# Performance work log

Measured on AMD Instinct MI355X. Metric: run time of the kernel, lower is better.

## Reference

```python
import jax, jax.numpy as jnp
import numpy as np
import math

B = 16
IMG = 224
P = 16
C_IN = 3
E = 768
H = 12
HD = E // H          # 64
D = 6                # depth
MLP = 3072
NC = 1000
GH = IMG // P        # 14
N = GH * GH + 1      # 197 tokens incl cls
LAMBDA_INIT = 0.8
EPS = 1e-5


def setup_inputs() -> dict:
    key = jax.random.key(0)
    ks = jax.random.split(key, 24)
    s = 0.02
    inp = {
        "x": jax.random.normal(ks[0], (B, C_IN, IMG, IMG), jnp.float32),
        "conv_w": jax.random.normal(ks[1], (E, C_IN, P, P), jnp.float32) * s,
        "conv_b": jnp.zeros((E,), jnp.float32),
        "cls_token": jax.random.normal(ks[2], (1, 1, E), jnp.float32) * s,
        "pos_embed": jax.random.normal(ks[3], (1, N, E), jnp.float32) * s,
        # per-layer stacked params (leading dim D)
        "Wq": jax.random.normal(ks[4], (D, E, 2 * E), jnp.float32) * s,
        "Wk": jax.random.normal(ks[5], (D, E, 2 * E), jnp.float32) * s,
        "Wv": jax.random.normal(ks[6], (D, E, 2 * E), jnp.float32) * s,
        "lq1": jax.random.normal(ks[7], (D, H, HD), jnp.float32) * 0.1,
        "lk1": jax.random.normal(ks[8], (D, H, HD), jnp.float32) * 0.1,
        "lq2": jax.random.normal(ks[9], (D, H, HD), jnp.float32) * 0.1,
        "lk2": jax.random.normal(ks[10], (D, H, HD), jnp.float32) * 0.1,
        "gn_g": jnp.ones((D, 2 * HD), jnp.float32),
        "gn_b": jnp.zeros((D, 2 * HD), jnp.float32),
        "Wo": jax.random.normal(ks[11], (D, 2 * E, E), jnp.float32) * s,
        "ln1_g": jnp.ones((D, E), jnp.float32),
        "ln1_b": jnp.zeros((D, E), jnp.float32),
        "ln2_g": jnp.ones((D, E), jnp.float32),
        "ln2_b": jnp.zeros((D, E), jnp.float32),
        "mlp_w1": jax.random.normal(ks[12], (D, E, MLP), jnp.float32) * s,
        "mlp_b1": jnp.zeros((D, MLP), jnp.float32),
        "mlp_w2": jax.random.normal(ks[13], (D, MLP, E), jnp.float32) * s,
        "mlp_b2": jnp.zeros((D, E), jnp.float32),
        "lnf_g": jnp.ones((E,), jnp.float32),
        "lnf_b": jnp.zeros((E,), jnp.float32),
        "head_w": jax.random.normal(ks[14], (E, NC), jnp.float32) * s,
        "head_b": jnp.zeros((NC,), jnp.float32),
    }
    return inp


def _ln(z, g, b):
    m = jnp.mean(z, axis=-1, keepdims=True)
    v = jnp.var(z, axis=-1, keepdims=True)
    return (z - m) * jax.lax.rsqrt(v + EPS) * g + b


def _forward(x, conv_w, conv_b, cls_token, pos_embed, Wq, Wk, Wv,
             lq1, lk1, lq2, lk2, gn_g, gn_b, Wo,
             ln1_g, ln1_b, ln2_g, ln2_b,
             mlp_w1, mlp_b1, mlp_w2, mlp_b2,
             lnf_g, lnf_b, head_w, head_b):
    Bx = x.shape[0]
    # patch embedding (conv stride=kernel == non-overlapping patch matmul)
    xp = x.reshape(Bx, C_IN, GH, P, GH, P)
    tok = jnp.einsum('bchpwq,ecpq->bhwe', xp, conv_w).reshape(Bx, GH * GH, E) + conv_b
    h = jnp.concatenate([jnp.broadcast_to(cls_token, (Bx, 1, E)), tok], axis=1) + pos_embed

    scale = 1.0 / math.sqrt(HD)

    def block(h, p):
        xn = _ln(h, p['ln1_g'], p['ln1_b'])
        q = (xn @ p['Wq']).reshape(Bx, N, H, 2 * HD).transpose(0, 2, 1, 3)
        k = (xn @ p['Wk']).reshape(Bx, N, H, 2 * HD).transpose(0, 2, 1, 3)
        v = (xn @ p['Wv']).reshape(Bx, N, H, 2 * HD).transpose(0, 2, 1, 3)
        q1, q2 = q[..., :HD], q[..., HD:]
        k1, k2 = k[..., :HD], k[..., HD:]
        a1 = jax.nn.softmax(jnp.einsum('bhnd,bhmd->bhnm', q1, k1) * scale, axis=-1)
        a2 = jax.nn.softmax(jnp.einsum('bhnd,bhmd->bhnm', q2, k2) * scale, axis=-1)
        lam = (jnp.exp(jnp.sum(p['lq1'] * p['lk1'], axis=-1))
               - jnp.exp(jnp.sum(p['lq2'] * p['lk2'], axis=-1)) + LAMBDA_INIT)  # (H,)
        attn = a1 - lam[None, :, None, None] * a2
        o = jnp.einsum('bhnm,bhmd->bhnd', attn, v)  # (B,H,N,2HD)
        # GroupNorm(1 group) over (N, 2HD) per (b,h) sample, per-channel affine
        m = jnp.mean(o, axis=(2, 3), keepdims=True)
        var = jnp.var(o, axis=(2, 3), keepdims=True)
        o = (o - m) * jax.lax.rsqrt(var + EPS) * p['gn_g'] + p['gn_b']
        o = o.transpose(0, 2, 1, 3).reshape(Bx, N, 2 * E) @ p['Wo']
        h = h + o
        xn2 = _ln(h, p['ln2_g'], p['ln2_b'])
        ff = jax.nn.gelu(xn2 @ p['mlp_w1'] + p['mlp_b1'], approximate=False) @ p['mlp_w2'] + p['mlp_b2']
        return h + ff, attn

    params = dict(Wq=Wq, Wk=Wk, Wv=Wv, lq1=lq1, lk1=lk1, lq2=lq2, lk2=lk2,
                  gn_g=gn_g, gn_b=gn_b, Wo=Wo, ln1_g=ln1_g, ln1_b=ln1_b,
                  ln2_g=ln2_g, ln2_b=ln2_b, mlp_w1=mlp_w1, mlp_b1=mlp_b1,
                  mlp_w2=mlp_w2, mlp_b2=mlp_b2)
    h, attns = jax.lax.scan(block, h, params)
    h = _ln(h, lnf_g, lnf_b)
    logits = h[:, 0] @ head_w + head_b
    return logits, attns  # attns: (D, B, H, N, N)


def reference(x, conv_w, conv_b, cls_token, pos_embed, Wq, Wk, Wv,
              lq1, lk1, lq2, lk2, gn_g, gn_b, Wo,
              ln1_g, ln1_b, ln2_g, ln2_b,
              mlp_w1, mlp_b1, mlp_w2, mlp_b2,
              lnf_g, lnf_b, head_w, head_b):
    return _forward(x, conv_w, conv_b, cls_token, pos_embed, Wq, Wk, Wv,
                    lq1, lk1, lq2, lk2, gn_g, gn_b, Wo,
                    ln1_g, ln1_b, ln2_g, ln2_b,
                    mlp_w1, mlp_b1, mlp_w2, mlp_b2,
                    lnf_g, lnf_b, head_w, head_b)
```

## Files before the change

### kernel.cpp

```cpp
#include <hip/hip_runtime.h>
#include <hip/hip_bf16.h>
#include <math.h>

#define BB 16
#define NT 197
#define EE 768
#define HH 12
#define E2 1536
#define MLPD 3072
#define NCLS 1000
#define ND 6
#define EPSF 1e-5f
#define SCALEF 0.125f
#define LAMINIT 0.8f
#define TOKC 3152

using v8bf  = __attribute__((ext_vector_type(8))) __bf16;
using f32x4 = __attribute__((ext_vector_type(4))) float;
typedef __hip_bfloat16 bf16;

#define AS1 __attribute__((address_space(1)))
#define AS3 __attribute__((address_space(3)))

__device__ __forceinline__ void gld16(const void* g, void* l) {
    __builtin_amdgcn_global_load_lds((const AS1 void*)g, (AS3 void*)l, 16, 0, 0);
}

__device__ __forceinline__ float gelu_f(float x) {
    const float u = x + 0.044715f * x * x * x;
    const float e = __expf(fminf(1.5957691216f * u, 80.f));
    return x * e / (e + 1.f);
}

__global__ __launch_bounds__(256) void gemm_bf16(
    const bf16* __restrict__ A, const bf16* __restrict__ Wt,
    const float* __restrict__ bias, float* __restrict__ C0,
    float* __restrict__ C1, float* __restrict__ C2,
    const float* __restrict__ pos, int M, int K, int ldA, int ldB, int Nc, int mode)
{
    __shared__ __align__(16) unsigned char smem[32768];
    const int t = threadIdx.x;
    const int wave = t >> 6, lane = t & 63;
    const int wr = wave >> 1, wc = wave & 1;
    const int lr = lane & 15, lk = lane >> 4;

    const int bid0 = blockIdx.y * gridDim.x + blockIdx.x;
    const int nwg = gridDim.x * gridDim.y;
    const int qv = nwg >> 3, rv = nwg & 7;
    const int xcd = bid0 & 7, ii = bid0 >> 3;
    const int wgid = (xcd < rv ? xcd * (qv + 1) : rv * (qv + 1) + (xcd - rv) * qv) + ii;
    const int rowBase = (wgid / gridDim.x) * 128;
    const int colBase = (wgid % gridDim.x) * 128;
    const size_t zoff = (size_t)blockIdx.z * K * 2;

    f32x4 acc[4][4];
#pragma unroll
    for (int i = 0; i < 4; ++i)
#pragma unroll
        for (int j = 0; j < 4; ++j) acc[i][j] = (f32x4){0.f,0.f,0.f,0.f};

    const size_t ldA2 = (size_t)ldA * 2, ldB2 = (size_t)ldB * 2;
    const int srow = t >> 3;
    const int schunk = (t & 7) ^ ((t >> 3) & 7);
    const char* Abase = (const char*)A + zoff + schunk * 16;
    const char* Bbase = (const char*)Wt + zoff + schunk * 16;
    unsigned char* lA = smem + t * 16;
    unsigned char* lB = smem + 16384 + t * 16;
    const v8bf* Sa = (const v8bf*)smem;
    const v8bf* Sb = (const v8bf*)(smem + 16384);

    int rA[4], rB[4];
#pragma unroll
    for (int c = 0; c < 4; ++c) {
        rA[c] = min(rowBase + c * 32 + srow, M - 1);
        rB[c] = colBase + c * 32 + srow;
    }

    for (int k0 = 0; k0 < K; k0 += 64) {
        const size_t kb = (size_t)k0 * 2;
#pragma unroll
        for (int c = 0; c < 4; ++c) {
            gld16(Abase + (size_t)rA[c] * ldA2 + kb, lA + c * 4096);
            gld16(Bbase + (size_t)rB[c] * ldB2 + kb, lB + c * 4096);
        }
        __syncthreads();
#pragma unroll
        for (int s = 0; s < 2; ++s) {
            const int xr_ = (s * 4 + lk) ^ (lr & 7);
            v8bf af[4], bfr[4];
#pragma unroll
            for (int i = 0; i < 4; ++i) af[i] = Sa[(wr * 64 + i * 16 + lr) * 8 + xr_];
#pragma unroll
            for (int j = 0; j < 4; ++j) bfr[j] = Sb[(wc * 64 + j * 16 + lr) * 8 + xr_];
#pragma unroll
            for (int i = 0; i < 4; ++i)
#pragma unroll
                for (int j = 0; j < 4; ++j)
                    acc[i][j] = __builtin_amdgcn_mfma_f32_16x16x32_bf16(af[i], bfr[j], acc[i][j], 0, 0, 0);
        }
        __syncthreads();
    }

    if (mode == 0) {
        float* Cs = (float*)smem;
        float* C0z = C0 + (size_t)blockIdx.z * M * Nc;
#pragma unroll
        for (int half = 0; half < 2; ++half) {
            __syncthreads();
            if (wr == half) {
#pragma unroll
                for (int i = 0; i < 4; ++i)
#pragma unroll
                    for (int j = 0; j < 4; ++j)
#pragma unroll
                        for (int rr = 0; rr < 4; ++rr)
                            Cs[(i*16 + lk*4 + rr)*128 + wc*64 + j*16 + lr] = acc[i][j][rr];
            }
            __syncthreads();
#pragma unroll
            for (int k = 0; k < 8; ++k) {
                const int idx = k*256 + t;
                const int row = idx >> 5, c4 = idx & 31;
                const int r = rowBase + half*64 + row;
                if (r < M)
                    *(float4*)&C0z[(size_t)r*Nc + colBase + c4*4] = *(float4*)&Cs[row*128 + c4*4];
            }
        }
    } else if (mode == 1) {
        const int which = colBase / E2;
        if (which == 2) {
#pragma unroll
            for (int i = 0; i < 4; ++i)
#pragma unroll
                for (int j = 0; j < 4; ++j)
#pragma unroll
                    for (int rr = 0; rr < 4; ++rr) {
                        const int r = rowBase + wr * 64 + i * 16 + lk * 4 + rr;
                        const int c = colBase + wc * 64 + j * 16 + lr;
                        if (r >= M) continue;
                        const int b_ = r / NT, n_ = r % NT;
                        const int cc = c % E2;
                        const int h_ = cc >> 7, d_ = cc & 127;
                        const size_t bh = (size_t)(b_ * HH + h_);
                        ((bf16*)C2)[((bh * 7 + (n_ >> 5)) * 8 + (d_ >> 4)) * 512 +
                                    (size_t)(((d_ & 15) + (((n_ >> 3) & 3) << 4)) * 8 + (n_ & 7))] =
                            __float2bfloat16(acc[i][j][rr]);
                    }
        } else {
            const int hFix = (colBase % E2) >> 7;
            bf16* dstBase = (bf16*)(which == 0 ? C0 : C1);
            bf16* Cs = (bf16*)smem;
            __syncthreads();
#pragma unroll
            for (int i = 0; i < 4; ++i)
#pragma unroll
                for (int j = 0; j < 4; ++j)
#pragma unroll
                    for (int rr = 0; rr < 4; ++rr)
                        Cs[(wr*64 + i*16 + lk*4 + rr)*128 + wc*64 + j*16 + lr] =
                            __float2bfloat16(acc[i][j][rr]);
            __syncthreads();
#pragma unroll
            for (int k = 0; k < 8; ++k) {
                const int idx = k*256 + t;
                const int row = idx >> 4, c8 = idx & 15;
                const int r = rowBase + row;
                if (r < M) {
                    const int b_ = r / NT, n_ = r - b_ * NT;
                    const size_t bh = (size_t)(b_ * HH + hFix);
                    *(uint4*)(dstBase + (bh * 208 + n_) * 128 + c8 * 8) =
                        *(uint4*)&Cs[row*128 + c8*8];
                }
            }
        }
    } else if (mode == 3) {
        bf16* Cs = (bf16*)smem;
        __syncthreads();
#pragma unroll
        for (int i = 0; i < 4; ++i)
#pragma unroll
            for (int j = 0; j < 4; ++j)
#pragma unroll
                for (int rr = 0; rr < 4; ++rr) {
                    const int c = colBase + wc*64 + j*16 + lr;
                    float val = acc[i][j][rr] + bias[c];
                    Cs[(wr*64 + i*16 + lk*4 + rr)*128 + wc*64 + j*16 + lr] =
                        __float2bfloat16(gelu_f(val));
                }
        __syncthreads();
        bf16* C0b = (bf16*)C0;
#pragma unroll
        for (int k = 0; k < 8; ++k) {
            const int idx = k*256 + t;
            const int row = idx >> 4, c8 = idx & 15;
            const int r = rowBase + row;
            if (r < M)
                *(uint4*)(C0b + (size_t)r*Nc + colBase + c8*8) = *(uint4*)&Cs[row*128 + c8*8];
        }
    } else {
#pragma unroll
        for (int i = 0; i < 4; ++i)
#pragma unroll
            for (int j = 0; j < 4; ++j)
#pragma unroll
                for (int rr = 0; rr < 4; ++rr) {
                    const int r = rowBase + wr * 64 + i * 16 + lk * 4 + rr;
                    const int c = colBase + wc * 64 + j * 16 + lr;
                    if (r >= M) continue;
                    const int b_ = r / 196, p_ = r % 196;
                    C0[((size_t)(b_ * NT) + 1 + p_) * EE + c] =
                        acc[i][j][rr] + bias[c] + pos[(size_t)(1 + p_) * EE + c];
                }
    }
}

__global__ __launch_bounds__(64) void attn_mfma(
    const bf16* __restrict__ Qrm, const bf16* __restrict__ Krm,
    const bf16* __restrict__ Vf, const float* __restrict__ lamp,
    float* __restrict__ aout, float* __restrict__ o, float* __restrict__ stats)
{
    const int lane = threadIdx.x;
    const int fid = blockIdx.x;
    const int xcd = fid & 7, rest = fid >> 3;
    const int qt = rest % 13, g = rest / 13;
    const int bh = g * 8 + xcd;
    const int hh = bh % HH;
    const int lr = lane & 15, lk = lane >> 4;

    __shared__ __align__(16) bf16 P[16][232];

    {
        const int r = lane & 15, c0 = 192 + (lane >> 4) * 10;
#pragma unroll
        for (int j = 0; j < 10; ++j) P[r][c0 + j] = __float2bfloat16(0.f);
    }

    v8bf qa[4];
    const bf16* Qb = Qrm + ((size_t)bh * 208 + qt * 16) * 128;
#pragma unroll
    for (int kk = 0; kk < 4; ++kk)
        qa[kk] = *(const v8bf*)(Qb + lr * 128 + kk * 32 + lk * 8);

    const bf16* Kb = Krm + (size_t)bh * 208 * 128;
    const f32x4 zf = {0.f, 0.f, 0.f, 0.f};
    f32x4 s1[13], s2[13];
#pragma unroll
    for (int t = 0; t < 13; ++t) {
        const bf16* Kt = Kb + (t * 16 + lr) * 128 + lk * 8;
        const v8bf k0 = *(const v8bf*)(Kt);
        const v8bf k1 = *(const v8bf*)(Kt + 32);
        const v8bf k2 = *(const v8bf*)(Kt + 64);
        const v8bf k3 = *(const v8bf*)(Kt + 96);
        s1[t] = __builtin_amdgcn_mfma_f32_16x16x32_bf16(qa[1], k1,
                __builtin_amdgcn_mfma_f32_16x16x32_bf16(qa[0], k0, zf, 0, 0, 0), 0, 0, 0);
        s2[t] = __builtin_amdgcn_mfma_f32_16x16x32_bf16(qa[3], k3,
                __builtin_amdgcn_mfma_f32_16x16x32_bf16(qa[2], k2, zf, 0, 0, 0), 0, 0, 0);
    }

    float m1[4] = {-1e30f,-1e30f,-1e30f,-1e30f}, m2[4] = {-1e30f,-1e30f,-1e30f,-1e30f};
#pragma unroll
    for (int t = 0; t < 13; ++t) {
        const bool kv = (t * 16 + lr) < NT;
#pragma unroll
        for (int rr = 0; rr < 4; ++rr) {
            s1[t][rr] = kv ? s1[t][rr] * SCALEF : -1e30f;
            s2[t][rr] = kv ? s2[t][rr] * SCALEF : -1e30f;
            m1[rr] = fmaxf(m1[rr], s1[t][rr]);
            m2[rr] = fmaxf(m2[rr], s2[t][rr]);
        }
    }
#pragma unroll
    for (int off = 8; off >= 1; off >>= 1)
#pragma unroll
        for (int rr = 0; rr < 4; ++rr) {
            m1[rr] = fmaxf(m1[rr], __shfl_xor(m1[rr], off));
            m2[rr] = fmaxf(m2[rr], __shfl_xor(m2[rr], off));
        }

    float z1[4] = {0,0,0,0}, z2[4] = {0,0,0,0};
#pragma unroll
    for (int t = 0; t < 13; ++t)
#pragma unroll
        for (int rr = 0; rr < 4; ++rr) {
            const float e1 = __expf(s1[t][rr] - m1[rr]);
            const float e2 = __expf(s2[t][rr] - m2[rr]);
            s1[t][rr] = e1; s2[t][rr] = e2;
            z1[rr] += e1; z2[rr] += e2;
        }
#pragma unroll
    for (int off = 8; off >= 1; off >>= 1)
#pragma unroll
        for (int rr = 0; rr < 4; ++rr) {
            z1[rr] += __shfl_xor(z1[rr], off);
            z2[rr] += __shfl_xor(z2[rr], off);
        }
    const float lam = lamp[hh];
    float r1[4], r2[4];
#pragma unroll
    for (int rr = 0; rr < 4; ++rr) { r1[rr] = 1.f / z1[rr]; r2[rr] = lam / z2[rr]; }

    __syncthreads();
#pragma unroll
    for (int t = 0; t < 13; ++t) {
        const int m_ = t * 16 + lr;
#pragma unroll
        for (int rr = 0; rr < 4; ++rr) {
            const float p = s1[t][rr] * r1[rr] - s2[t][rr] * r2[rr];
            const int n_ = lk * 4 + rr;
            P[n_][m_] = __float2bfloat16(p);
            const int n_g = qt * 16 + n_;
            if (m_ < NT && n_g < NT)
                aout[((size_t)bh * NT + n_g) * NT + m_] = p;
        }
    }
    __syncthreads();

    f32x4 oacc[8];
#pragma unroll
    for (int dt = 0; dt < 8; ++dt) oacc[dt] = zf;
    const v8bf* Vp = (const v8bf*)(Vf + (size_t)bh * 7 * 8 * 512);
    const bf16* Pb = &P[0][0];
#pragma unroll
    for (int mk = 0; mk < 7; ++mk) {
        const v8bf pa = *(const v8bf*)(Pb + lr * 232 + mk * 32 + lk * 8);
#pragma unroll
        for (int dt = 0; dt < 8; ++dt)
            oacc[dt] = __builtin_amdgcn_mfma_f32_16x16x32_bf16(
                pa, Vp[(mk * 8 + dt) * 64 + lane], oacc[dt], 0, 0, 0);
    }
#pragma unroll
    for (int dt = 0; dt < 8; ++dt)
#pragma unroll
        for (int rr = 0; rr < 4; ++rr) {
            const int n_g = qt * 16 + lk * 4 + rr;
            if (n_g < NT)
                o[((size_t)bh * NT + n_g) * 128 + dt * 16 + lr] = oacc[dt][rr];
        }

    float s = 0.f, ss = 0.f;
#pragma unroll
    for (int dt = 0; dt < 8; ++dt)
#pragma unroll
        for (int rr = 0; rr < 4; ++rr) {
            const int n_g = qt * 16 + lk * 4 + rr;
            const float vv = (n_g < NT) ? oacc[dt][rr] : 0.f;
            s += vv; ss += vv * vv;
        }
#pragma unroll
    for (int off = 32; off >= 1; off >>= 1) {
        s  += __shfl_xor(s, off);
        ss += __shfl_xor(ss, off);
    }
    if (lane == 0) {
        stats[(bh * 13 + qt) * 2]     = s;
        stats[(bh * 13 + qt) * 2 + 1] = ss;
    }
}

__global__ __launch_bounds__(256) void gn_apply(
    const float* __restrict__ o, const float* __restrict__ stats,
    const float* __restrict__ g, const float* __restrict__ bb, bf16* __restrict__ o2)
{
    const int bh = blockIdx.y, qq = blockIdx.x;
    const int t = threadIdx.x;
    float S = 0.f, SS = 0.f;
#pragma unroll
    for (int j = 0; j < 13; ++j) {
        S  += stats[(bh * 13 + j) * 2];
        SS += stats[(bh * 13 + j) * 2 + 1];
    }
    const float inv = 1.f / (float)(NT * 128);
    const float mean = S * inv;
    const float var  = SS * inv - mean * mean;
    const float rstd = rsqrtf(var + EPSF);
    const int b_ = bh / HH, h_ = bh % HH;
    const float4* ob = (const float4*)(o + (size_t)bh * NT * 128);
    const float4* g4 = (const float4*)g;
    const float4* b4 = (const float4*)bb;
    for (int idx = t; idx < 50 * 32; idx += 256) {
        const int n_ = qq * 50 + (idx >> 5);
        if (n_ >= NT) continue;
        const int d4 = idx & 31;
        const float4 v4 = ob[n_ * 32 + d4];
        const float4 gg = g4[d4], bv = b4[d4];
        bf16 tmp[4];
        tmp[0] = __float2bfloat16((v4.x - mean) * rstd * gg.x + bv.x);
        tmp[1] = __float2bfloat16((v4.y - mean) * rstd * gg.y + bv.y);
        tmp[2] = __float2bfloat16((v4.z - mean) * rstd * gg.z + bv.z);
        tmp[3] = __float2bfloat16((v4.w - mean) * rstd * gg.w + bv.w);
        *(uint2*)(o2 + ((size_t)(b_ * NT + n_)) * E2 + h_ * 128 + d4 * 4) = *(uint2*)tmp;
    }
}

__global__ __launch_bounds__(256) void ln_rows(
    const float* __restrict__ in, const float* __restrict__ g,
    const float* __restrict__ bb, bf16* __restrict__ out)
{
    const int r = blockIdx.x;
    const int t = threadIdx.x;
    const float* x = in + (size_t)r * EE;
    const float v0 = x[t], v1 = x[t+256], v2 = x[t+512];
    __shared__ float rs[256], rss[256];
    rs[t]  = v0+v1+v2;
    rss[t] = v0*v0+v1*v1+v2*v2;
    __syncthreads();
    for (int st = 128; st > 0; st >>= 1) {
        if (t < st) { rs[t] += rs[t+st]; rss[t] += rss[t+st]; }
        __syncthreads();
    }
    const float mean = rs[0] * (1.f/768.f);
    const float var  = rss[0] * (1.f/768.f) - mean*mean;
    const float rstd = rsqrtf(var + EPSF);
    bf16* o = out + (size_t)r * EE;
    o[t]     = __float2bfloat16((v0-mean)*rstd*g[t]     + bb[t]);
    o[t+256] = __float2bfloat16((v1-mean)*rstd*g[t+256] + bb[t+256]);
    o[t+512] = __float2bfloat16((v2-mean)*rstd*g[t+512] + bb[t+512]);
}

__global__ __launch_bounds__(192) void ln_fuse(
    const float* __restrict__ hin, const float* __restrict__ Pp,
    const float* __restrict__ bias, const float* __restrict__ g,
    const float* __restrict__ bb, float* __restrict__ hout, bf16* __restrict__ xout)
{
    const int r = blockIdx.x;
    const int t = threadIdx.x;
    const int lane = t & 63, wv = t >> 6;
    const size_t base4 = (size_t)r * 192 + t;
    float4 v = ((const float4*)hin)[base4];
    const float4 p0 = ((const float4*)Pp)[base4];
    const float4 p1 = ((const float4*)Pp)[(size_t)TOKC * 192 + base4];
    v.x += p0.x + p1.x; v.y += p0.y + p1.y; v.z += p0.z + p1.z; v.w += p0.w + p1.w;
    if (bias) {
        const float4 bv = ((const float4*)bias)[t];
        v.x += bv.x; v.y += bv.y; v.z += bv.z; v.w += bv.w;
    }
    float s  = v.x + v.y + v.z + v.w;
    float ss = v.x*v.x + v.y*v.y + v.z*v.z + v.w*v.w;
#pragma unroll
    for (int off = 32; off >= 1; off >>= 1) {
        s  += __shfl_xor(s, off);
        ss += __shfl_xor(ss, off);
    }
    __shared__ float ws_[3][2];
    if (lane == 0) { ws_[wv][0] = s; ws_[wv][1] = ss; }
    __syncthreads();
    const float S  = ws_[0][0] + ws_[1][0] + ws_[2][0];
    const float SS = ws_[0][1] + ws_[1][1] + ws_[2][1];
    const float mean = S * (1.f/768.f);
    const float var  = SS * (1.f/768.f) - mean*mean;
    const float rstd = rsqrtf(var + EPSF);
    ((float4*)hout)[base4] = v;
    const float4 gg = ((const float4*)g)[t];
    const float4 bv2 = ((const float4*)bb)[t];
    bf16 tmp[4];
    tmp[0] = __float2bfloat16((v.x-mean)*rstd*gg.x + bv2.x);
    tmp[1] = __float2bfloat16((v.y-mean)*rstd*gg.y + bv2.y);
    tmp[2] = __float2bfloat16((v.z-mean)*rstd*gg.z + bv2.z);
    tmp[3] = __float2bfloat16((v.w-mean)*rstd*gg.w + bv2.w);
    *(uint2*)(xout + base4 * 4) = *(uint2*)tmp;
}

__global__ void lam_kernel(const float* __restrict__ lq1, const float* __restrict__ lk1,
                           const float* __restrict__ lq2, const float* __restrict__ lk2,
                           float* __restrict__ lam)
{
    const int i = threadIdx.x;
    if (i < ND*HH) {
        float d1 = 0.f, d2 = 0.f;
        for (int d = 0; d < 64; ++d) {
            d1 += lq1[i*64+d]*lk1[i*64+d];
            d2 += lq2[i*64+d]*lk2[i*64+d];
        }
        lam[i] = expf(d1) - expf(d2) + LAMINIT;
    }
}

__global__ void cls_kernel(const float* __restrict__ cls, const float* __restrict__ pos,
                           float* __restrict__ h)
{
    const int i = blockIdx.x*256 + threadIdx.x;
    if (i < BB*EE) {
        const int b_ = i / EE, e_ = i % EE;
        h[(size_t)(b_*NT)*EE + e_] = cls[e_] + pos[e_];
    }
}

__global__ void im2col_kernel(const float* __restrict__ x, bf16* __restrict__ xcol)
{
    const int i = blockIdx.x*256 + threadIdx.x;
    if (i >= 3136*EE) return;
    const int kidx = i % EE;
    const int p_ = i / EE;
    const int b_ = p_ / 196;
    const int pp = p_ % 196;
    const int gh = pp / 14, gw = pp % 14;
    const int c_ = kidx >> 8, rr = (kidx >> 4) & 15, q_ = kidx & 15;
    xcol[i] = __float2bfloat16(x[((size_t)(b_*3 + c_)*224 + gh*16 + rr)*224 + gw*16 + q_]);
}

__global__ void convert_flat(const float* __restrict__ in, bf16* __restrict__ out, int n)
{
    const int i = blockIdx.x*256 + threadIdx.x;
    if (i < n) out[i] = __float2bfloat16(in[i]);
}

__global__ void transpose_pack(const float* __restrict__ Wq, const float* __restrict__ Wk,
                               const float* __restrict__ Wv, const float* __restrict__ Wo,
                               const float* __restrict__ W1, const float* __restrict__ W2,
                               bf16* __restrict__ wall)
{
    __shared__ float tile[64][65];
    int bid = blockIdx.x;
    const int dl = bid / 2304; bid -= dl * 2304;
    bf16* wq_t = wall + (size_t)dl * 9437184;
    bf16* wo_t = wq_t + 3538944;
    bf16* w1_t = wo_t + 1179648;
    bf16* w2_t = w1_t + 2359296;
    const float* src; bf16* dst; int K, N, gx;
    if (bid < 864) {
        const int z = bid / 288; bid -= z * 288;
        src = (z == 0 ? Wq : (z == 1 ? Wk : Wv)) + (size_t)dl * EE * E2;
        dst = wq_t + (size_t)z * E2 * EE; K = EE; N = E2; gx = 24;
    } else if (bid < 1152) { src = Wo + (size_t)dl*E2*EE; dst = wo_t; K = E2; N = EE; gx = 12; bid -= 864; }
    else if (bid < 1728)   { src = W1 + (size_t)dl*EE*MLPD; dst = w1_t; K = EE; N = MLPD; gx = 48; bid -= 1152; }
    else                   { src = W2 + (size_t)dl*MLPD*EE; dst = w2_t; K = MLPD; N = EE; gx = 12; bid -= 1728; }
    const int bx = bid % gx, by = bid / gx;
    const int t = threadIdx.x;
    const int n0 = bx*64, k0 = by*64;
    {
        const int c4 = t & 15, kr = t >> 4;
#pragma unroll
        for (int i = 0; i < 4; ++i) {
            const int row = i * 16 + kr;
            const float4 v = *(const float4*)(src + (size_t)(k0 + row) * N + n0 + c4 * 4);
            tile[row][c4*4+0] = v.x; tile[row][c4*4+1] = v.y;
            tile[row][c4*4+2] = v.z; tile[row][c4*4+3] = v.w;
        }
    }
    __syncthreads();
    {
        const int ko = t & 7, nb = t >> 3;
#pragma unroll
        for (int i = 0; i < 2; ++i) {
            const int n = i * 32 + nb;
            bf16 tmp[8];
#pragma unroll
            for (int j = 0; j < 8; ++j)
                tmp[j] = __float2bfloat16(tile[ko*8+j][n]);
            *(uint4*)(dst + (size_t)(n0 + n) * K + k0 + ko * 8) = *(uint4*)tmp;
        }
    }
}

__global__ __launch_bounds__(256) void ln_cls(
    const float* __restrict__ h, const float* __restrict__ g,
    const float* __restrict__ bb, float* __restrict__ xr)
{
    const int b_ = blockIdx.x;
    const int t = threadIdx.x;
    const float* x = h + (size_t)(b_*NT)*EE;
    const float v0 = x[t], v1 = x[t+256], v2 = x[t+512];
    __shared__ float rs[256], rss[256];
    rs[t]  = v0+v1+v2;
    rss[t] = v0*v0+v1*v1+v2*v2;
    __syncthreads();
    for (int st = 128; st > 0; st >>= 1) {
        if (t < st) { rs[t] += rs[t+st]; rss[t] += rss[t+st]; }
        __syncthreads();
    }
    const float mean = rs[0] * (1.f/768.f);
    const float var  = rss[0] * (1.f/768.f) - mean*mean;
    const float rstd = rsqrtf(var + EPSF);
    float* o = xr + (size_t)b_ * EE;
    o[t]     = (v0-mean)*rstd*g[t]     + bb[t];
    o[t+256] = (v1-mean)*rstd*g[t+256] + bb[t+256];
    o[t+512] = (v2-mean)*rstd*g[t+512] + bb[t+512];
}

__global__ __launch_bounds__(256) void head_gemm(
    const float* __restrict__ xr, const float* __restrict__ hw,
    const float* __restrict__ hb, float* __restrict__ logits)
{
    const int b_ = blockIdx.y, ct = blockIdx.x;
    const int t = threadIdx.x;
    const int c_loc = t & 63, kp = t >> 6;
    const int c = ct * 64 + c_loc;
    __shared__ float xs[768];
    for (int i = t; i < 768; i += 256) xs[i] = xr[(size_t)b_*EE + i];
    __syncthreads();
    float acc = 0.f;
    if (c < NCLS) {
        const int k0 = kp * 192;
        for (int kk = k0; kk < k0 + 192; ++kk)
            acc += xs[kk] * hw[(size_t)kk * NCLS + c];
    }
    __shared__ float red[4][64];
    red[kp][c_loc] = acc;
    __syncthreads();
    if (kp == 0 && c < NCLS)
        logits[(size_t)b_*NCLS + c] =
            red[0][c_loc] + red[1][c_loc] + red[2][c_loc] + red[3][c_loc] + hb[c];
}

extern "C" void kernel_launch(void* const* d_in, const int* in_sizes, int n_in,
                              void* d_out, int out_size, void* d_ws, size_t ws_size,
                              hipStream_t stream)
{
    const float* x      = (const float*)d_in[0];
    const float* conv_w = (const float*)d_in[1];
    const float* conv_b = (const float*)d_in[2];
    const float* cls    = (const float*)d_in[3];
    const float* pos    = (const float*)d_in[4];
    const float* Wq     = (const float*)d_in[5];
    const float* Wk     = (const float*)d_in[6];
    const float* Wv     = (const float*)d_in[7];
    const float* lq1    = (const float*)d_in[8];
    const float* lk1    = (const float*)d_in[9];
    const float* lq2    = (const float*)d_in[10];
    const float* lk2    = (const float*)d_in[11];
    const float* gn_g   = (const float*)d_in[12];
    const float* gn_b   = (const float*)d_in[13];
    const float* Wo     = (const float*)d_in[14];
    const float* ln1_g  = (const float*)d_in[15];
    const float* ln1_b  = (const float*)d_in[16];
    const float* ln2_g  = (const float*)d_in[17];
    const float* ln2_b  = (const float*)d_in[18];
    const float* mlp_w1 = (const float*)d_in[19];
    const float* mlp_b1 = (const float*)d_in[20];
    const float* mlp_w2 = (const float*)d_in[21];
    const float* mlp_b2 = (const float*)d_in[22];
    const float* lnf_g  = (const float*)d_in[23];
    const float* lnf_b  = (const float*)d_in[24];
    const float* head_w = (const float*)d_in[25];
    const float* head_b = (const float*)d_in[26];

    float* out_f    = (float*)d_out;
    float* logits   = out_f;
    float* attn_out = out_f + (size_t)BB*NCLS;

    const int TOK = TOKC;
    const size_t TOKE = (size_t)TOK*EE;

    float* ws   = (float*)d_ws;
    float* h    = ws;
    float* o    = h + TOKE;
    float* Pp   = o + (size_t)BB*HH*NT*128;
    bf16*  Qrm  = (bf16*)(Pp + 2*TOKE);
    bf16*  Krm  = Qrm + (size_t)192*208*128;
    bf16*  Vf   = Krm + (size_t)192*208*128;
    bf16*  act2 = Vf + (size_t)192*7*8*512;
    bf16*  xn   = act2 + (size_t)TOK*MLPD;
    bf16*  wall = xn + TOKE;
    bf16*  cwbf = wall + (size_t)6*9437184;
    float* lam  = (float*)(cwbf + (size_t)EE*EE);
    float* xr   = lam + 128;
    float* gnst = xr + (size_t)BB*EE;

    hipMemsetAsync(Vf, 0, (size_t)192*7*8*512*2, stream);

    lam_kernel<<<1, 128, 0, stream>>>(lq1, lk1, lq2, lk2, lam);
    convert_flat<<<(EE*EE+255)/256, 256, 0, stream>>>(conv_w, cwbf, EE*EE);
    transpose_pack<<<6*2304, 256, 0, stream>>>(Wq, Wk, Wv, Wo, mlp_w1, mlp_w2, wall);
    im2col_kernel<<<(3136*EE+255)/256, 256, 0, stream>>>(x, xn);
    cls_kernel<<<(BB*EE+255)/256, 256, 0, stream>>>(cls, pos, h);
    gemm_bf16<<<dim3(EE/128, 25), 256, 0, stream>>>(
        xn, cwbf, conv_b, h, nullptr, nullptr, pos, 3136, EE, EE, EE, EE, 4);

    ln_rows<<<TOK, 256, 0, stream>>>(h, ln1_g, ln1_b, xn);

    for (int dl = 0; dl < ND; ++dl) {
        bf16* wq_t = wall + (size_t)dl*9437184;
        bf16* wo_t = wq_t + 3538944;
        bf16* w1_t = wo_t + 1179648;
        bf16* w2_t = w1_t + 2359296;

        gemm_bf16<<<dim3(4608/128, 25), 256, 0, stream>>>(
            xn, wq_t, nullptr, (float*)Qrm, (float*)Krm, (float*)Vf, nullptr,
            TOK, EE, EE, EE, 4608, 1);
        attn_mfma<<<2496, 64, 0, stream>>>(
            Qrm, Krm, Vf, lam + dl*HH, attn_out + (size_t)dl*BB*HH*NT*NT, o, gnst);
        gn_apply<<<dim3(4, BB*HH), 256, 0, stream>>>(
            o, gnst, gn_g + dl*128, gn_b + dl*128, act2);
        gemm_bf16<<<dim3(EE/128, 25, 2), 256, 0, stream>>>(
            act2, wo_t, nullptr, Pp, nullptr, nullptr, nullptr,
            TOK, E2/2, E2, E2, EE, 0);
        ln_fuse<<<TOK, 192, 0, stream>>>(
            h, Pp, nullptr, ln2_g + dl*EE, ln2_b + dl*EE, h, xn);
        gemm_bf16<<<dim3(MLPD/128, 25), 256, 0, stream>>>(
            xn, w1_t, mlp_b1 + dl*MLPD, (float*)act2, nullptr, nullptr, nullptr,
            TOK, EE, EE, EE, MLPD, 3);
        gemm_bf16<<<dim3(EE/128, 25, 2), 256, 0, stream>>>(
            act2, w2_t, nullptr, Pp, nullptr, nullptr, nullptr,
            TOK, MLPD/2, MLPD, MLPD, EE, 0);
        if (dl < ND-1)
            ln_fuse<<<TOK, 192, 0, stream>>>(
                h, Pp, mlp_b2 + dl*EE, ln1_g + (dl+1)*EE, ln1_b + (dl+1)*EE, h, xn);
        else
            ln_fuse<<<TOK, 192, 0, stream>>>(
                h, Pp, mlp_b2 + dl*EE, lnf_g, lnf_b, h, xn);
    }

    ln_cls<<<BB, 256, 0, stream>>>(h, lnf_g, lnf_b, xr);
    head_gemm<<<dim3(16, BB), 256, 0, stream>>>(xr, head_w, head_b, logits);
}
```

Measured before the change: 1.492 ms.

## Add 256x256-tile bf16 GEMM kernel for QKV and MLP-up projections

Introduces a new 512-thread GEMM kernel with 256x256 output tiles, double-buffered LDS holding 64-wide K slices, an XCD-aware workgroup remap, and split MFMA phases with s_setprio. It replaces the 128-tile GEMM for the QKV projection and the first MLP layer, keeping the fused QKV scatter and bias+GELU epilogues. The larger tiles aim to improve operand reuse and cut global traffic per FLOP. In exchange the grid has far fewer workgroups (13x18 or 13x12), so CU occupancy and wave-quantization behaviour change, and the 128KB of LDS per block limits residency.

```diff
diff --git a/kernel.cpp b/kernel.cpp
--- a/kernel.cpp
+++ b/kernel.cpp
@@ -211,6 +211,201 @@
                     C0[((size_t)(b_ * NT) + 1 + p_) * EE + c] =
                         acc[i][j][rr] + bias[c] + pos[(size_t)(1 + p_) * EE + c];
                 }
+    }
+}
+
+__global__ __launch_bounds__(512, 2) void gemm256(
+    const bf16* __restrict__ A, const bf16* __restrict__ Wt,
+    const float* __restrict__ bias, float* __restrict__ C0,
+    float* __restrict__ C1, float* __restrict__ C2,
+    int M, int K, int Nc, int mode)
+{
+    __shared__ __align__(16) unsigned char smem[131072];
+    const int t = threadIdx.x;
+    const int wave = t >> 6, lane = t & 63;
+    const int wm = wave >> 2, wn = wave & 3;
+    const int lr = lane & 15, lk = lane >> 4;
+
+    const int bid0 = blockIdx.y * gridDim.x + blockIdx.x;
+    const int nwg = gridDim.x * gridDim.y;
+    const int qv = nwg >> 3, rv = nwg & 7;
+    const int xcd = bid0 & 7, ii = bid0 >> 3;
+    const int wgid = (xcd < rv ? xcd * (qv + 1) : rv * (qv + 1) + (xcd - rv) * qv) + ii;
+    const int rowBase = (wgid / gridDim.x) * 256;
+    const int colBase = (wgid % gridDim.x) * 256;
+
+    f32x4 acc[8][4];
+#pragma unroll
+    for (int i = 0; i < 8; ++i)
+#pragma unroll
+        for (int j = 0; j < 4; ++j) acc[i][j] = (f32x4){0.f,0.f,0.f,0.f};
+
+    const size_t ldK2 = (size_t)K * 2;
+    const int srow = t >> 3;
+    const int schunk = (t & 7) ^ (srow & 7);
+    const char* Abase = (const char*)A + schunk * 16;
+    const char* Bbase = (const char*)Wt + schunk * 16;
+
+    int rA[4], rB[4];
+#pragma unroll
+    for (int p = 0; p < 4; ++p) {
+        rA[p] = min(rowBase + p * 64 + srow, M - 1);
+        rB[p] = colBase + p * 64 + srow;
+    }
+
+    {
+        unsigned char* l0 = smem + t * 16;
+#pragma unroll
+        for (int p = 0; p < 4; ++p) {
+            gld16(Abase + (size_t)rA[p] * ldK2, l0 + p * 8192);
+            gld16(Bbase + (size_t)rB[p] * ldK2, l0 + 32768 + p * 8192);
+        }
+#pragma unroll
+        for (int p = 0; p < 4; ++p) {
+            gld16(Abase + (size_t)rA[p] * ldK2 + 128, l0 + 65536 + p * 8192);
+            gld16(Bbase + (size_t)rB[p] * ldK2 + 128, l0 + 65536 + 32768 + p * 8192);
+        }
+        asm volatile("s_waitcnt vmcnt(8)" ::: "memory");
+        asm volatile("s_barrier" ::: "memory");
+    }
+
+    const int NTt = K >> 6;
+    for (int kt = 0; kt < NTt; ++kt) {
+        const int buf = kt & 1;
+        const v8bf* Sa = (const v8bf*)(smem + buf * 65536);
+        const v8bf* Sb = (const v8bf*)(smem + buf * 65536 + 32768);
+
+        v8bf bfr[2][4], af[2][4];
+#pragma unroll
+        for (int s = 0; s < 2; ++s) {
+            const int x0 = s * 4 + lk;
+#pragma unroll
+            for (int j = 0; j < 4; ++j) {
+                const int row = wn * 64 + j * 16 + lr;
+                bfr[s][j] = Sb[row * 8 + (x0 ^ (lr & 7))];
+            }
+#pragma unroll
+            for (int i = 0; i < 4; ++i) {
+                const int row = wm * 128 + i * 16 + lr;
+                af[s][i] = Sa[row * 8 + (x0 ^ (lr & 7))];
+            }
+        }
+        __builtin_amdgcn_s_setprio(1);
+#pragma unroll
+        for (int s = 0; s < 2; ++s)
+#pragma unroll
+            for (int i = 0; i < 4; ++i)
+#pragma unroll
+                for (int j = 0; j < 4; ++j)
+                    acc[i][j] = __builtin_amdgcn_mfma_f32_16x16x32_bf16(af[s][i], bfr[s][j], acc[i][j], 0, 0, 0);
+        __builtin_amdgcn_s_setprio(0);
+
+        v8bf af2[2][4];
+#pragma unroll
+        for (int s = 0; s < 2; ++s)
+#pragma unroll
+            for (int i = 0; i < 4; ++i) {
+                const int row = wm * 128 + 64 + i * 16 + lr;
+                af2[s][i] = Sa[row * 8 + ((s * 4 + lk) ^ (lr & 7))];
+            }
+        asm volatile("s_waitcnt lgkmcnt(0)" ::: "memory");
+        asm volatile("s_barrier" ::: "memory");
+        if (kt + 2 < NTt) {
+            const size_t kb = (size_t)(kt + 2) * 128;
+            unsigned char* ld = smem + buf * 65536 + t * 16;
+#pragma unroll
+            for (int p = 0; p < 4; ++p) {
+                gld16(Abase + (size_t)rA[p] * ldK2 + kb, ld + p * 8192);
+                gld16(Bbase + (size_t)rB[p] * ldK2 + kb, ld + 32768 + p * 8192);
+            }
+            asm volatile("s_waitcnt vmcnt(8)" ::: "memory");
+        } else {
+            asm volatile("s_waitcnt vmcnt(0)" ::: "memory");
+        }
+        asm volatile("s_barrier" ::: "memory");
+        __builtin_amdgcn_s_setprio(1);
+#pragma unroll
+        for (int s = 0; s < 2; ++s)
+#pragma unroll
+            for (int i = 0; i < 4; ++i)
+#pragma unroll
+                for (int j = 0; j < 4; ++j)
+                    acc[4 + i][j] = __builtin_amdgcn_mfma_f32_16x16x32_bf16(af2[s][i], bfr[s][j], acc[4 + i][j], 0, 0, 0);
+        __builtin_amdgcn_s_setprio(0);
+    }
+
+    if (mode == 1) {
+        const int which = colBase / E2;
+        if (which == 2) {
+#pragma unroll
+            for (int i = 0; i < 8; ++i)
+#pragma unroll
+                for (int j = 0; j < 4; ++j)
+#pragma unroll
+                    for (int rr = 0; rr < 4; ++rr) {
+                        const int r = rowBase + wm * 128 + i * 16 + lk * 4 + rr;
+                        if (r >= M) continue;
+                        const int c = colBase + wn * 64 + j * 16 + lr;
+                        const int b_ = r / NT, n_ = r % NT;
+                        const int cc = c % E2;
+                        const int h_ = cc >> 7, d_ = cc & 127;
+                        const size_t bh = (size_t)(b_ * HH + h_);
+                        ((bf16*)C2)[((bh * 7 + (n_ >> 5)) * 8 + (d_ >> 4)) * 512 +
+                                    (size_t)(((d_ & 15) + (((n_ >> 3) & 3) << 4)) * 8 + (n_ & 7))] =
+                            __float2bfloat16(acc[i][j][rr]);
+                    }
+        } else {
+            bf16* dstBase = (bf16*)(which == 0 ? C0 : C1);
+            const int h0 = (colBase % E2) >> 7;
+            bf16* Cs = (bf16*)smem;
+            __syncthreads();
+#pragma unroll
+            for (int i = 0; i < 8; ++i)
+#pragma unroll
+                for (int j = 0; j < 4; ++j)
+#pragma unroll
+                    for (int rr = 0; rr < 4; ++rr)
+                        Cs[(wm*128 + i*16 + lk*4 + rr)*256 + wn*64 + j*16 + lr] =
+                            __float2bfloat16(acc[i][j][rr]);
+            __syncthreads();
+#pragma unroll
+            for (int k = 0; k < 16; ++k) {
+                const int idx = k * 512 + t;
+                const int row = idx >> 5, c8 = idx & 31;
+                const int r = rowBase + row;
+                if (r < M) {
+                    const int b_ = r / NT, n_ = r - b_ * NT;
+                    const size_t bh = (size_t)(b_ * HH + h0 + (c8 >> 4));
+                    *(uint4*)(dstBase + (bh * 208 + n_) * 128 + (size_t)(c8 & 15) * 8) =
+                        *(uint4*)&Cs[row * 256 + c8 * 8];
+                }
+            }
+        }
+    } else {
+        bf16* Cs = (bf16*)smem;
+        __syncthreads();
+#pragma unroll
+        for (int i = 0; i < 8; ++i)
+#pragma unroll
+            for (int j = 0; j < 4; ++j) {
+                const int c = colBase + wn * 64 + j * 16 + lr;
+                const float bv = bias[c];
+#pragma unroll
+                for (int rr = 0; rr < 4; ++rr)
+                    Cs[(wm*128 + i*16 + lk*4 + rr)*256 + wn*64 + j*16 + lr] =
+                        __float2bfloat16(gelu_f(acc[i][j][rr] + bv));
+            }
+        __syncthreads();
+        bf16* C0b = (bf16*)C0;
+#pragma unroll
+        for (int k = 0; k < 16; ++k) {
+            const int idx = k * 512 + t;
+            const int row = idx >> 5, c8 = idx & 31;
+            const int r = rowBase + row;
+            if (r < M)
+                *(uint4*)(C0b + (size_t)r * Nc + colBase + c8 * 8) =
+                    *(uint4*)&Cs[row * 256 + c8 * 8];
+        }
     }
 }
 
@@ -674,9 +869,9 @@
         bf16* w1_t = wo_t + 1179648;
         bf16* w2_t = w1_t + 2359296;
 
-        gemm_bf16<<<dim3(4608/128, 25), 256, 0, stream>>>(
-            xn, wq_t, nullptr, (float*)Qrm, (float*)Krm, (float*)Vf, nullptr,
-            TOK, EE, EE, EE, 4608, 1);
+        gemm256<<<dim3(4608/256, (TOK+255)/256), 512, 0, stream>>>(
+            xn, wq_t, nullptr, (float*)Qrm, (float*)Krm, (float*)Vf,
+            TOK, EE, 4608, 1);
         attn_mfma<<<2496, 64, 0, stream>>>(
             Qrm, Krm, Vf, lam + dl*HH, attn_out + (size_t)dl*BB*HH*NT*NT, o, gnst);
         gn_apply<<<dim3(4, BB*HH), 256, 0, stream>>>(
@@ -686,9 +881,9 @@
             TOK, E2/2, E2, E2, EE, 0);
         ln_fuse<<<TOK, 192, 0, stream>>>(
             h, Pp, nullptr, ln2_g + dl*EE, ln2_b + dl*EE, h, xn);
-        gemm_bf16<<<dim3(MLPD/128, 25), 256, 0, stream>>>(
-            xn, w1_t, mlp_b1 + dl*MLPD, (float*)act2, nullptr, nullptr, nullptr,
-            TOK, EE, EE, EE, MLPD, 3);
+        gemm256<<<dim3(MLPD/256, (TOK+255)/256), 512, 0, stream>>>(
+            xn, w1_t, mlp_b1 + dl*MLPD, (float*)act2, nullptr, nullptr,
+            TOK, EE, MLPD, 3);
         gemm_bf16<<<dim3(EE/128, 25, 2), 256, 0, stream>>>(
             act2, w2_t, nullptr, Pp, nullptr, nullptr, nullptr,
             TOK, MLPD/2, MLPD, MLPD, EE, 0);
```

New measurement: 1.437 ms. 3.7% less time.
